# Optimization experiments

Hardware: AMD Instinct MI355X
Metric: run time of the kernel (lower is better)

## Reference

```python
import jax, jax.numpy as jnp
import numpy as np

N = 100_000          # nodes
E = 3_200_000        # edges (avg degree 32)
EMB = 16             # item embedding dim
IN = EMB + 1         # concat(embed, scalar feature)
HID = 32             # GAT hidden size
NEMB = 1000          # embedding vocab
SLOPE = 0.2          # GATConv leaky_relu negative slope


def setup_inputs() -> dict:
    key = jax.random.key(0)
    ks = jax.random.split(key, 24)
    g = lambda k, shape, fan: jax.random.normal(k, shape, dtype=jnp.float32) * (1.0 / np.sqrt(fan))
    inp = {
        "x_ids": jax.random.randint(ks[0], (N,), 0, NEMB, dtype=jnp.int32),
        "x_feat": jax.random.normal(ks[1], (N, 1), dtype=jnp.float32),
        "src": jax.random.randint(ks[2], (E,), 0, N, dtype=jnp.int32),
        "dst": jax.random.randint(ks[3], (E,), 0, N, dtype=jnp.int32),
        "edge_attr": jax.random.normal(ks[4], (E, 1), dtype=jnp.float32),
        # embedding table
        "emb": g(ks[5], (NEMB, EMB), EMB),
        # GATConv 1 (in=17, out=32, heads=1, edge_dim=1)
        "W1": g(ks[6], (IN, HID), IN),
        "a_s1": g(ks[7], (HID,), HID),
        "a_d1": g(ks[8], (HID,), HID),
        "We1": g(ks[9], (1, HID), 1),
        "a_e1": g(ks[10], (HID,), HID),
        "b1": jnp.zeros((HID,), jnp.float32),
        # GATConv 2 (in=32, out=32)
        "W2": g(ks[11], (HID, HID), HID),
        "a_s2": g(ks[12], (HID,), HID),
        "a_d2": g(ks[13], (HID,), HID),
        "We2": g(ks[14], (1, HID), 1),
        "a_e2": g(ks[15], (HID,), HID),
        "b2": jnp.zeros((HID,), jnp.float32),
        # final linear (32 -> 1)
        "lin_w": g(ks[16], (HID, 1), HID),
        "lin_b": jnp.zeros((1,), jnp.float32),
    }
    return inp


def _gat_conv(x, src, dst, eattr, W, a_s, a_d, We, a_e, b):
    """PyG GATConv (heads=1, concat=True) with edge features, self-loops already added."""
    h = x @ W                                   # [N, HID]
    alpha_src = h @ a_s                         # [N]
    alpha_dst = h @ a_d                         # [N]
    alpha_edge = (eattr @ We) @ a_e             # [E']
    alpha = jax.nn.leaky_relu(alpha_src[src] + alpha_dst[dst] + alpha_edge, SLOPE)
    # segment softmax over incoming edges of each dst node
    m = jax.ops.segment_max(alpha, dst, num_segments=N)
    ex = jnp.exp(alpha - m[dst])
    denom = jax.ops.segment_sum(ex, dst, num_segments=N)
    coef = ex / (denom[dst] + 1e-16)
    out = jax.ops.segment_sum(coef[:, None] * h[src], dst, num_segments=N)
    return out + b


def reference(x_ids, x_feat, src, dst, edge_attr, emb,
              W1, a_s1, a_d1, We1, a_e1, b1,
              W2, a_s2, a_d2, We2, a_e2, b2,
              lin_w, lin_b):
    # embedding lookup + concat scalar feature -> [N, 17]
    x = jnp.concatenate([emb[x_ids], x_feat], axis=1)

    # add self-loops once; self-loop edge_attr = mean of incoming edge attrs (fill_value='mean')
    loop = jnp.arange(N, dtype=src.dtype)
    deg = jax.ops.segment_sum(jnp.ones((E,), x.dtype), dst, num_segments=N)
    loop_attr = jax.ops.segment_sum(edge_attr, dst, num_segments=N) / jnp.maximum(deg, 1.0)[:, None]
    src2 = jnp.concatenate([src, loop])
    dst2 = jnp.concatenate([dst, loop])
    ea2 = jnp.concatenate([edge_attr, loop_attr], axis=0)

    x = _gat_conv(x, src2, dst2, ea2, W1, a_s1, a_d1, We1, a_e1, b1)
    x = jax.nn.relu(x)  # dropout is identity in eval mode
    x = _gat_conv(x, src2, dst2, ea2, W2, a_s2, a_d2, We2, a_e2, b2)
    return x @ lin_w + lin_b  # [N, 1]
```

## Files before the change

kernel.cpp:

```cpp
#include <hip/hip_runtime.h>

#define NN 100000
#define EE 3200000
#define SLOPE 0.2f

#define BKN 128
constexpr int NBK = (NN + BKN - 1) / BKN;
#define CAP 4544
constexpr int EP = EE + NN;
#define EPB 4096
constexpr int NBB = (EE + EPB - 1) / EPB;

__global__ void k_bucket(const int* __restrict__ src, const int* __restrict__ dst,
                         const float* __restrict__ ea, int* __restrict__ cnt,
                         int2* __restrict__ stage) {
    __shared__ int hst[NBK];
    __shared__ int scl[NBK];
    __shared__ int gdel[NBK];
    __shared__ int aux[256];
    __shared__ int2 rec[EPB];
    __shared__ int addr[EPB];
    int t = threadIdx.x;
    int base = blockIdx.x * EPB;
    int nedge = min(EPB, EE - base);
    for (int i = t; i < NBK; i += 256) hst[i] = 0;
    __syncthreads();
    int ds[16], ss[16]; float es[16];
#pragma unroll
    for (int j = 0; j < 16; j++) {
        int e = base + j * 256 + t;
        bool v = e < EE;
        ds[j] = v ? dst[e] : -1;
        ss[j] = v ? src[e] : 0;
        es[j] = v ? ea[e] : 0.f;
        if (v) atomicAdd(&hst[ds[j] >> 7], 1);
    }
    __syncthreads();
    int i0 = t * 4;
    int v0 = (i0 + 0 < NBK) ? hst[i0 + 0] : 0;
    int v1 = (i0 + 1 < NBK) ? hst[i0 + 1] : 0;
    int v2 = (i0 + 2 < NBK) ? hst[i0 + 2] : 0;
    int v3 = (i0 + 3 < NBK) ? hst[i0 + 3] : 0;
    int tsum = v0 + v1 + v2 + v3;
    aux[t] = tsum;
    __syncthreads();
    for (int off = 1; off < 256; off <<= 1) {
        int x = (t >= off) ? aux[t - off] : 0;
        __syncthreads();
        aux[t] += x;
        __syncthreads();
    }
    int ex = aux[t] - tsum;
    if (i0 + 0 < NBK) scl[i0 + 0] = ex;
    if (i0 + 1 < NBK) scl[i0 + 1] = ex + v0;
    if (i0 + 2 < NBK) scl[i0 + 2] = ex + v0 + v1;
    if (i0 + 3 < NBK) scl[i0 + 3] = ex + v0 + v1 + v2;
    __syncthreads();
    for (int i = t; i < NBK; i += 256) {
        int h = hst[i];
        int g = h ? atomicAdd(&cnt[i], h) : 0;
        gdel[i] = (g + i * CAP) - scl[i];
    }
    __syncthreads();
#pragma unroll
    for (int j = 0; j < 16; j++) {
        if (ds[j] >= 0) {
            int bk = ds[j] >> 7;
            int pos = atomicAdd(&scl[bk], 1);
            int gpos = pos + gdel[bk];
            rec[pos] = make_int2(ss[j] | ((ds[j] & 127) << 17), __float_as_int(es[j]));
            addr[pos] = (gpos - bk * CAP < CAP) ? gpos : -1;
        }
    }
    __syncthreads();
    for (int i = t; i < nedge; i += 256) {
        int a = addr[i];
        if (a >= 0) stage[a] = rec[i];
    }
}

__global__ void k_scanb(const int* __restrict__ cnt, int* __restrict__ fbase) {
    __shared__ int a[1024];
    int t = threadIdx.x;
    int v = 0;
    if (t < NBK) v = min(cnt[t], CAP) + min(BKN, NN - t * BKN);
    a[t] = v;
    __syncthreads();
    for (int off = 1; off < 1024; off <<= 1) {
        int x = (t >= off) ? a[t - off] : 0;
        __syncthreads();
        a[t] += x;
        __syncthreads();
    }
    if (t < NBK) fbase[t] = a[t] - v;
}

__global__ void k_build(const int* __restrict__ cnt, const int* __restrict__ fbase,
                        const int2* __restrict__ stage, int2* __restrict__ csr,
                        int* __restrict__ offs) {
    __shared__ int ldeg[BKN];
    __shared__ float esum[BKN];
    __shared__ int sc[BKN];
    __shared__ int lcur[BKN];
    int b = blockIdx.x, t = threadIdx.x;
    int nbase = b * BKN;
    int npb = min(BKN, NN - nbase);
    int c = min(cnt[b], CAP);
    const int2* ep = stage + (size_t)b * CAP;
    if (t < BKN) { ldeg[t] = 0; esum[t] = 0.f; }
    __syncthreads();
    for (int i = t; i < c; i += 256) {
        int2 e = ep[i];
        int n = (e.x >> 17) & 127;
        atomicAdd(&ldeg[n], 1);
        atomicAdd(&esum[n], __int_as_float(e.y));
    }
    __syncthreads();
    int v = (t < npb) ? ldeg[t] + 1 : 0;
    if (t < BKN) sc[t] = v;
    __syncthreads();
    for (int off = 1; off < BKN; off <<= 1) {
        int x = (t >= off && t < BKN) ? sc[t - off] : 0;
        __syncthreads();
        if (t < BKN) sc[t] += x;
        __syncthreads();
    }
    if (t < npb) {
        int start = fbase[b] + sc[t] - v;
        offs[nbase + t] = start;
        lcur[t] = start;
    }
    __syncthreads();
    for (int i = t; i < c; i += 256) {
        int2 e = ep[i];
        int n = (e.x >> 17) & 127;
        int pos = atomicAdd(&lcur[n], 1);
        csr[pos] = make_int2(e.x & 0x1FFFF, e.y);
    }
    __syncthreads();
    if (t < npb) {
        float mean = esum[t] / fmaxf((float)ldeg[t], 1.0f);
        csr[lcur[t]] = make_int2(nbase + t, __float_as_int(mean));
    }
    if (b == 0 && t == 0) offs[NN] = EP;
}

__global__ void k_const(const float* __restrict__ We1, const float* __restrict__ ae1,
                        const float* __restrict__ We2, const float* __restrict__ ae2,
                        float* __restrict__ cbuf) {
    int lane = threadIdx.x & 63;
    int comp = lane & 31;
    float p = (lane < 32) ? We1[comp] * ae1[comp] : We2[comp] * ae2[comp];
#pragma unroll
    for (int off = 16; off >= 1; off >>= 1) p += __shfl_xor(p, off);
    if (comp == 0) cbuf[lane >> 5] = p;
}


__global__ void k_h1(const int* __restrict__ ids, const float* __restrict__ feat,
                     const float* __restrict__ emb, const float* __restrict__ W,
                     const float* __restrict__ avs, const float* __restrict__ avd,
                     float* __restrict__ h, float* __restrict__ as_, float* __restrict__ ad_) {
    int n = blockIdx.x * 256 + threadIdx.x;
    if (n >= NN) return;
    float hv[32];
#pragma unroll
    for (int j = 0; j < 32; j++) hv[j] = 0.f;
    int id = ids[n];
    const float4* e4 = (const float4*)(emb + (size_t)id * 16);
#pragma unroll
    for (int k4 = 0; k4 < 4; k4++) {
        float4 xv = e4[k4];
        const float* wr = W + k4 * 4 * 32;
#pragma unroll
        for (int j = 0; j < 32; j++)
            hv[j] += xv.x * wr[j] + xv.y * wr[32 + j] + xv.z * wr[64 + j] + xv.w * wr[96 + j];
    }
    float f = feat[n];
#pragma unroll
    for (int j = 0; j < 32; j++) hv[j] += f * W[16 * 32 + j];
    float s = 0.f, d = 0.f;
#pragma unroll
    for (int j = 0; j < 32; j++) { s += hv[j] * avs[j]; d += hv[j] * avd[j]; }
    as_[n] = s;
    ad_[n] = d;
    float4* h4 = (float4*)(h + (size_t)n * 32);
#pragma unroll
    for (int q = 0; q < 8; q++)
        h4[q] = make_float4(hv[4 * q], hv[4 * q + 1], hv[4 * q + 2], hv[4 * q + 3]);
}

__global__ void k_h2(const float* __restrict__ x, const float* __restrict__ W,
                     const float* __restrict__ avs, const float* __restrict__ avd,
                     float* __restrict__ h, float* __restrict__ as_, float* __restrict__ ad_) {
    int n = blockIdx.x * 256 + threadIdx.x;
    if (n >= NN) return;
    float hv[32];
#pragma unroll
    for (int j = 0; j < 32; j++) hv[j] = 0.f;
    const float4* x4 = (const float4*)(x + (size_t)n * 32);
#pragma unroll
    for (int k4 = 0; k4 < 8; k4++) {
        float4 xv = x4[k4];
        const float* wr = W + k4 * 4 * 32;
#pragma unroll
        for (int j = 0; j < 32; j++)
            hv[j] += xv.x * wr[j] + xv.y * wr[32 + j] + xv.z * wr[64 + j] + xv.w * wr[96 + j];
    }
    float s = 0.f, d = 0.f;
#pragma unroll
    for (int j = 0; j < 32; j++) { s += hv[j] * avs[j]; d += hv[j] * avd[j]; }
    as_[n] = s;
    ad_[n] = d;
    float4* h4 = (float4*)(h + (size_t)n * 32);
#pragma unroll
    for (int q = 0; q < 8; q++)
        h4[q] = make_float4(hv[4 * q], hv[4 * q + 1], hv[4 * q + 2], hv[4 * q + 3]);
}

template <bool FINAL>
__global__ void k_gat(const int* __restrict__ offs, const int2* __restrict__ csr,
                      const float* __restrict__ h, const float* __restrict__ as_,
                      const float* __restrict__ ad_, const float* __restrict__ cbuf,
                      int cidx, const float* __restrict__ bias,
                      const float* __restrict__ lw, const float* __restrict__ lb,
                      float* __restrict__ out) {
    __shared__ int2 xb[4][64];
    int wid = threadIdx.x >> 6;
    int node = blockIdx.x * 4 + wid;
    if (node >= NN) return;
    int lane = threadIdx.x & 63;
    int comp = lane & 31;
    int slot = lane >> 5;
    int base = offs[node];
    int cnt = offs[node + 1] - base;
    float c = cbuf[cidx];
    float adn = ad_[node];
    float acc0 = 0.f, acc1 = 0.f, acc2 = 0.f, acc3 = 0.f, exs = 0.f;
    for (int cb = 0; cb < cnt; cb += 64) {
        int idx = cb + lane;
        bool val = idx < cnt;
        int2 e = csr[base + (val ? idx : 0)];
        int s = e.x;
        float a = as_[s] + adn + c * __int_as_float(e.y);
        a = (a >= 0.f) ? a : SLOPE * a;
        float ex = val ? __expf(a) : 0.f;
        exs += ex;
        xb[wid][lane] = make_int2(s << 5, __float_as_int(ex));
        int m = min(cnt - cb, 64);
        for (int j = 0; j < m; j += 8) {
            int2 p0 = xb[wid][j + slot];
            int2 p1 = xb[wid][j + 2 + slot];
            int2 p2 = xb[wid][j + 4 + slot];
            int2 p3 = xb[wid][j + 6 + slot];
            acc0 += __int_as_float(p0.y) * h[p0.x + comp];
            acc1 += __int_as_float(p1.y) * h[p1.x + comp];
            acc2 += __int_as_float(p2.y) * h[p2.x + comp];
            acc3 += __int_as_float(p3.y) * h[p3.x + comp];
        }
    }
    float acc = (acc0 + acc1) + (acc2 + acc3);
    acc += __shfl_xor(acc, 32);
#pragma unroll
    for (int off = 1; off < 64; off <<= 1) exs += __shfl_xor(exs, off);
    float o = acc / (exs + 1e-16f) + bias[comp];
    if (!FINAL) {
        o = fmaxf(o, 0.f);
        if (lane < 32) out[(size_t)node * 32 + comp] = o;
    } else {
        float y = o * lw[comp];
#pragma unroll
        for (int off = 16; off >= 1; off >>= 1) y += __shfl_xor(y, off);
        if (lane == 0) out[node] = y + lb[0];
    }
}


extern "C" void kernel_launch(void* const* d_in, const int* in_sizes, int n_in,
                              void* d_out, int out_size, void* d_ws, size_t ws_size,
                              hipStream_t stream) {
    const int* x_ids = (const int*)d_in[0];
    const float* x_feat = (const float*)d_in[1];
    const int* src = (const int*)d_in[2];
    const int* dst = (const int*)d_in[3];
    const float* eattr = (const float*)d_in[4];
    const float* emb = (const float*)d_in[5];
    const float* W1 = (const float*)d_in[6];
    const float* a_s1 = (const float*)d_in[7];
    const float* a_d1 = (const float*)d_in[8];
    const float* We1 = (const float*)d_in[9];
    const float* a_e1 = (const float*)d_in[10];
    const float* b1 = (const float*)d_in[11];
    const float* W2 = (const float*)d_in[12];
    const float* a_s2 = (const float*)d_in[13];
    const float* a_d2 = (const float*)d_in[14];
    const float* We2 = (const float*)d_in[15];
    const float* a_e2 = (const float*)d_in[16];
    const float* b2 = (const float*)d_in[17];
    const float* lin_w = (const float*)d_in[18];
    const float* lin_b = (const float*)d_in[19];

    char* p = (char*)d_ws;
    auto alloc = [&](size_t bytes) {
        void* r = (void*)p;
        p += (bytes + 255) & ~(size_t)255;
        return r;
    };
    int* cnt = (int*)alloc(NBK * 4);
    int* fbase = (int*)alloc(NBK * 4);
    float* cbuf = (float*)alloc(2 * 4);
    int* offs = (int*)alloc((NN + 1) * 4);
    float* asb = (float*)alloc(NN * 4);
    float* adb = (float*)alloc(NN * 4);
    int2* csr = (int2*)alloc((size_t)EP * 8);
    void* regionA = alloc((size_t)NBK * CAP * 8);
    int2* stage = (int2*)regionA;
    float* hbuf = (float*)regionA;
    float* x2 = hbuf + (size_t)NN * 32;
    (void)ws_size; (void)in_sizes; (void)n_in; (void)out_size;

    hipMemsetAsync(cnt, 0, NBK * 4, stream);

    const int NBT = (NN + 255) / 256;
    const int NW = (NN + 3) / 4;

    k_bucket<<<NBB, 256, 0, stream>>>(src, dst, eattr, cnt, stage);
    k_scanb<<<1, 1024, 0, stream>>>(cnt, fbase);
    k_build<<<NBK, 256, 0, stream>>>(cnt, fbase, stage, csr, offs);
    k_const<<<1, 64, 0, stream>>>(We1, a_e1, We2, a_e2, cbuf);

    k_h1<<<NBT, 256, 0, stream>>>(x_ids, x_feat, emb, W1, a_s1, a_d1, hbuf, asb, adb);
    k_gat<false><<<NW, 256, 0, stream>>>(offs, csr, hbuf, asb, adb, cbuf, 0, b1,
                                         nullptr, nullptr, x2);
    k_h2<<<NBT, 256, 0, stream>>>(x2, W2, a_s2, a_d2, hbuf, asb, adb);
    k_gat<true><<<NW, 256, 0, stream>>>(offs, csr, hbuf, asb, adb, cbuf, 1, b2,
                                        lin_w, lin_b, (float*)d_out);
}
```

Measured before the change: 352.5 us.

## Fuse node projections into bucketing and GAT kernels, merge small launches

```diff
diff --git a/kernel.cpp b/kernel.cpp
--- a/kernel.cpp
+++ b/kernel.cpp
@@ -10,10 +10,16 @@
 constexpr int EP = EE + NN;
 #define EPB 4096
 constexpr int NBB = (EE + EPB - 1) / EPB;
-
-__global__ void k_bucket(const int* __restrict__ src, const int* __restrict__ dst,
-                         const float* __restrict__ ea, int* __restrict__ cnt,
-                         int2* __restrict__ stage) {
+constexpr int NBT = (NN + 255) / 256;
+
+__global__ void k_fat(const int* __restrict__ src, const int* __restrict__ dst,
+                      const float* __restrict__ ea, int* __restrict__ cnt,
+                      int2* __restrict__ stage,
+                      const int* __restrict__ ids, const float* __restrict__ feat,
+                      const float* __restrict__ emb, const float* __restrict__ W,
+                      const float* __restrict__ avs, const float* __restrict__ avd,
+                      float* __restrict__ h, float* __restrict__ as_,
+                      float* __restrict__ ad_) {
     __shared__ int hst[NBK];
     __shared__ int scl[NBK];
     __shared__ int gdel[NBK];
@@ -21,67 +27,110 @@
     __shared__ int2 rec[EPB];
     __shared__ int addr[EPB];
     int t = threadIdx.x;
-    int base = blockIdx.x * EPB;
-    int nedge = min(EPB, EE - base);
-    for (int i = t; i < NBK; i += 256) hst[i] = 0;
-    __syncthreads();
-    int ds[16], ss[16]; float es[16];
-#pragma unroll
-    for (int j = 0; j < 16; j++) {
-        int e = base + j * 256 + t;
-        bool v = e < EE;
-        ds[j] = v ? dst[e] : -1;
-        ss[j] = v ? src[e] : 0;
-        es[j] = v ? ea[e] : 0.f;
-        if (v) atomicAdd(&hst[ds[j] >> 7], 1);
-    }
-    __syncthreads();
-    int i0 = t * 4;
-    int v0 = (i0 + 0 < NBK) ? hst[i0 + 0] : 0;
-    int v1 = (i0 + 1 < NBK) ? hst[i0 + 1] : 0;
-    int v2 = (i0 + 2 < NBK) ? hst[i0 + 2] : 0;
-    int v3 = (i0 + 3 < NBK) ? hst[i0 + 3] : 0;
-    int tsum = v0 + v1 + v2 + v3;
-    aux[t] = tsum;
-    __syncthreads();
-    for (int off = 1; off < 256; off <<= 1) {
-        int x = (t >= off) ? aux[t - off] : 0;
-        __syncthreads();
-        aux[t] += x;
-        __syncthreads();
-    }
-    int ex = aux[t] - tsum;
-    if (i0 + 0 < NBK) scl[i0 + 0] = ex;
-    if (i0 + 1 < NBK) scl[i0 + 1] = ex + v0;
-    if (i0 + 2 < NBK) scl[i0 + 2] = ex + v0 + v1;
-    if (i0 + 3 < NBK) scl[i0 + 3] = ex + v0 + v1 + v2;
-    __syncthreads();
-    for (int i = t; i < NBK; i += 256) {
-        int h = hst[i];
-        int g = h ? atomicAdd(&cnt[i], h) : 0;
-        gdel[i] = (g + i * CAP) - scl[i];
-    }
-    __syncthreads();
-#pragma unroll
-    for (int j = 0; j < 16; j++) {
-        if (ds[j] >= 0) {
-            int bk = ds[j] >> 7;
-            int pos = atomicAdd(&scl[bk], 1);
-            int gpos = pos + gdel[bk];
-            rec[pos] = make_int2(ss[j] | ((ds[j] & 127) << 17), __float_as_int(es[j]));
-            addr[pos] = (gpos - bk * CAP < CAP) ? gpos : -1;
-        }
-    }
-    __syncthreads();
-    for (int i = t; i < nedge; i += 256) {
-        int a = addr[i];
-        if (a >= 0) stage[a] = rec[i];
-    }
-}
-
-__global__ void k_scanb(const int* __restrict__ cnt, int* __restrict__ fbase) {
+    if (blockIdx.x < NBB) {
+        int base = blockIdx.x * EPB;
+        int nedge = min(EPB, EE - base);
+        for (int i = t; i < NBK; i += 256) hst[i] = 0;
+        __syncthreads();
+        int ds[16], ss[16]; float es[16];
+#pragma unroll
+        for (int j = 0; j < 16; j++) {
+            int e = base + j * 256 + t;
+            bool v = e < EE;
+            ds[j] = v ? dst[e] : -1;
+            ss[j] = v ? src[e] : 0;
+            es[j] = v ? ea[e] : 0.f;
+            if (v) atomicAdd(&hst[ds[j] >> 7], 1);
+        }
+        __syncthreads();
+        int i0 = t * 4;
+        int v0 = (i0 + 0 < NBK) ? hst[i0 + 0] : 0;
+        int v1 = (i0 + 1 < NBK) ? hst[i0 + 1] : 0;
+        int v2 = (i0 + 2 < NBK) ? hst[i0 + 2] : 0;
+        int v3 = (i0 + 3 < NBK) ? hst[i0 + 3] : 0;
+        int tsum = v0 + v1 + v2 + v3;
+        aux[t] = tsum;
+        __syncthreads();
+        for (int off = 1; off < 256; off <<= 1) {
+            int x = (t >= off) ? aux[t - off] : 0;
+            __syncthreads();
+            aux[t] += x;
+            __syncthreads();
+        }
+        int ex = aux[t] - tsum;
+        if (i0 + 0 < NBK) scl[i0 + 0] = ex;
+        if (i0 + 1 < NBK) scl[i0 + 1] = ex + v0;
+        if (i0 + 2 < NBK) scl[i0 + 2] = ex + v0 + v1;
+        if (i0 + 3 < NBK) scl[i0 + 3] = ex + v0 + v1 + v2;
+        __syncthreads();
+        for (int i = t; i < NBK; i += 256) {
+            int hh = hst[i];
+            int g = hh ? atomicAdd(&cnt[i], hh) : 0;
+            gdel[i] = (g + i * CAP) - scl[i];
+        }
+        __syncthreads();
+#pragma unroll
+        for (int j = 0; j < 16; j++) {
+            if (ds[j] >= 0) {
+                int bk = ds[j] >> 7;
+                int pos = atomicAdd(&scl[bk], 1);
+                int gpos = pos + gdel[bk];
+                rec[pos] = make_int2(ss[j] | ((ds[j] & 127) << 17), __float_as_int(es[j]));
+                addr[pos] = (gpos - bk * CAP < CAP) ? gpos : -1;
+            }
+        }
+        __syncthreads();
+        for (int i = t; i < nedge; i += 256) {
+            int a = addr[i];
+            if (a >= 0) stage[a] = rec[i];
+        }
+    } else {
+        int n = (blockIdx.x - NBB) * 256 + t;
+        if (n >= NN) return;
+        float hv[32];
+#pragma unroll
+        for (int j = 0; j < 32; j++) hv[j] = 0.f;
+        int id = ids[n];
+        const float4* e4 = (const float4*)(emb + (size_t)id * 16);
+#pragma unroll
+        for (int k4 = 0; k4 < 4; k4++) {
+            float4 xv = e4[k4];
+            const float* wr = W + k4 * 4 * 32;
+#pragma unroll
+            for (int j = 0; j < 32; j++)
+                hv[j] += xv.x * wr[j] + xv.y * wr[32 + j] + xv.z * wr[64 + j] + xv.w * wr[96 + j];
+        }
+        float f = feat[n];
+#pragma unroll
+        for (int j = 0; j < 32; j++) hv[j] += f * W[16 * 32 + j];
+        float s = 0.f, d = 0.f;
+#pragma unroll
+        for (int j = 0; j < 32; j++) { s += hv[j] * avs[j]; d += hv[j] * avd[j]; }
+        as_[n] = s;
+        ad_[n] = d;
+        float4* h4 = (float4*)(h + (size_t)n * 32);
+#pragma unroll
+        for (int q = 0; q < 8; q++)
+            h4[q] = make_float4(hv[4 * q], hv[4 * q + 1], hv[4 * q + 2], hv[4 * q + 3]);
+    }
+}
+
+__global__ void k_scanc(const int* __restrict__ cnt, int* __restrict__ fbase,
+                        const float* __restrict__ We1, const float* __restrict__ ae1,
+                        const float* __restrict__ We2, const float* __restrict__ ae2,
+                        float* __restrict__ cbuf) {
     __shared__ int a[1024];
     int t = threadIdx.x;
+    if (blockIdx.x == 1) {
+        if (t < 64) {
+            int comp = t & 31;
+            float p = (t < 32) ? We1[comp] * ae1[comp] : We2[comp] * ae2[comp];
+#pragma unroll
+            for (int off = 16; off >= 1; off >>= 1) p += __shfl_xor(p, off);
+            if (comp == 0) cbuf[t >> 5] = p;
+        }
+        return;
+    }
     int v = 0;
     if (t < NBK) v = min(cnt[t], CAP) + min(BKN, NN - t * BKN);
     a[t] = v;
@@ -109,7 +158,7 @@
     const int2* ep = stage + (size_t)b * CAP;
     if (t < BKN) { ldeg[t] = 0; esum[t] = 0.f; }
     __syncthreads();
-    for (int i = t; i < c; i += 256) {
+    for (int i = t; i < c; i += 1024) {
         int2 e = ep[i];
         int n = (e.x >> 17) & 127;
         atomicAdd(&ldeg[n], 1);
@@ -131,7 +180,7 @@
         lcur[t] = start;
     }
     __syncthreads();
-    for (int i = t; i < c; i += 256) {
+    for (int i = t; i < c; i += 1024) {
         int2 e = ep[i];
         int n = (e.x >> 17) & 127;
         int pos = atomicAdd(&lcur[n], 1);
@@ -143,79 +192,6 @@
         csr[lcur[t]] = make_int2(nbase + t, __float_as_int(mean));
     }
     if (b == 0 && t == 0) offs[NN] = EP;
-}
-
-__global__ void k_const(const float* __restrict__ We1, const float* __restrict__ ae1,
-                        const float* __restrict__ We2, const float* __restrict__ ae2,
-                        float* __restrict__ cbuf) {
-    int lane = threadIdx.x & 63;
-    int comp = lane & 31;
-    float p = (lane < 32) ? We1[comp] * ae1[comp] : We2[comp] * ae2[comp];
-#pragma unroll
-    for (int off = 16; off >= 1; off >>= 1) p += __shfl_xor(p, off);
-    if (comp == 0) cbuf[lane >> 5] = p;
-}
-
-
-__global__ void k_h1(const int* __restrict__ ids, const float* __restrict__ feat,
-                     const float* __restrict__ emb, const float* __restrict__ W,
-                     const float* __restrict__ avs, const float* __restrict__ avd,
-                     float* __restrict__ h, float* __restrict__ as_, float* __restrict__ ad_) {
-    int n = blockIdx.x * 256 + threadIdx.x;
-    if (n >= NN) return;
-    float hv[32];
-#pragma unroll
-    for (int j = 0; j < 32; j++) hv[j] = 0.f;
-    int id = ids[n];
-    const float4* e4 = (const float4*)(emb + (size_t)id * 16);
-#pragma unroll
-    for (int k4 = 0; k4 < 4; k4++) {
-        float4 xv = e4[k4];
-        const float* wr = W + k4 * 4 * 32;
-#pragma unroll
-        for (int j = 0; j < 32; j++)
-            hv[j] += xv.x * wr[j] + xv.y * wr[32 + j] + xv.z * wr[64 + j] + xv.w * wr[96 + j];
-    }
-    float f = feat[n];
-#pragma unroll
-    for (int j = 0; j < 32; j++) hv[j] += f * W[16 * 32 + j];
-    float s = 0.f, d = 0.f;
-#pragma unroll
-    for (int j = 0; j < 32; j++) { s += hv[j] * avs[j]; d += hv[j] * avd[j]; }
-    as_[n] = s;
-    ad_[n] = d;
-    float4* h4 = (float4*)(h + (size_t)n * 32);
-#pragma unroll
-    for (int q = 0; q < 8; q++)
-        h4[q] = make_float4(hv[4 * q], hv[4 * q + 1], hv[4 * q + 2], hv[4 * q + 3]);
-}
-
-__global__ void k_h2(const float* __restrict__ x, const float* __restrict__ W,
-                     const float* __restrict__ avs, const float* __restrict__ avd,
-                     float* __restrict__ h, float* __restrict__ as_, float* __restrict__ ad_) {
-    int n = blockIdx.x * 256 + threadIdx.x;
-    if (n >= NN) return;
-    float hv[32];
-#pragma unroll
-    for (int j = 0; j < 32; j++) hv[j] = 0.f;
-    const float4* x4 = (const float4*)(x + (size_t)n * 32);
-#pragma unroll
-    for (int k4 = 0; k4 < 8; k4++) {
-        float4 xv = x4[k4];
-        const float* wr = W + k4 * 4 * 32;
-#pragma unroll
-        for (int j = 0; j < 32; j++)
-            hv[j] += xv.x * wr[j] + xv.y * wr[32 + j] + xv.z * wr[64 + j] + xv.w * wr[96 + j];
-    }
-    float s = 0.f, d = 0.f;
-#pragma unroll
-    for (int j = 0; j < 32; j++) { s += hv[j] * avs[j]; d += hv[j] * avd[j]; }
-    as_[n] = s;
-    ad_[n] = d;
-    float4* h4 = (float4*)(h + (size_t)n * 32);
-#pragma unroll
-    for (int q = 0; q < 8; q++)
-        h4[q] = make_float4(hv[4 * q], hv[4 * q + 1], hv[4 * q + 2], hv[4 * q + 3]);
 }
 
 template <bool FINAL>
@@ -223,20 +199,29 @@
                       const float* __restrict__ h, const float* __restrict__ as_,
                       const float* __restrict__ ad_, const float* __restrict__ cbuf,
                       int cidx, const float* __restrict__ bias,
+                      const float* __restrict__ W2, const float* __restrict__ avs2,
+                      const float* __restrict__ avd2, float* __restrict__ h2,
+                      float* __restrict__ as2, float* __restrict__ ad2,
                       const float* __restrict__ lw, const float* __restrict__ lb,
                       float* __restrict__ out) {
     __shared__ int2 xb[4][64];
-    int wid = threadIdx.x >> 6;
+    __shared__ float w2s[1024];
+    int t = threadIdx.x;
+    if (!FINAL) {
+        for (int i = t; i < 1024; i += 256) w2s[i] = W2[i];
+        __syncthreads();
+    }
+    int wid = t >> 6;
     int node = blockIdx.x * 4 + wid;
-    if (node >= NN) return;
-    int lane = threadIdx.x & 63;
-    int comp = lane & 31;
-    int slot = lane >> 5;
+    int lane = t & 63;
+    int comp = t & 31;
+    int slot = (t >> 5) & 1;
     int base = offs[node];
     int cnt = offs[node + 1] - base;
     float c = cbuf[cidx];
     float adn = ad_[node];
-    float acc0 = 0.f, acc1 = 0.f, acc2 = 0.f, acc3 = 0.f, exs = 0.f;
+    float a0 = 0.f, a1 = 0.f, a2 = 0.f, a3 = 0.f;
+    float a4 = 0.f, a5 = 0.f, a6 = 0.f, a7 = 0.f, exs = 0.f;
     for (int cb = 0; cb < cnt; cb += 64) {
         int idx = cb + lane;
         bool val = idx < cnt;
@@ -248,25 +233,45 @@
         exs += ex;
         xb[wid][lane] = make_int2(s << 5, __float_as_int(ex));
         int m = min(cnt - cb, 64);
-        for (int j = 0; j < m; j += 8) {
-            int2 p0 = xb[wid][j + slot];
-            int2 p1 = xb[wid][j + 2 + slot];
-            int2 p2 = xb[wid][j + 4 + slot];
-            int2 p3 = xb[wid][j + 6 + slot];
-            acc0 += __int_as_float(p0.y) * h[p0.x + comp];
-            acc1 += __int_as_float(p1.y) * h[p1.x + comp];
-            acc2 += __int_as_float(p2.y) * h[p2.x + comp];
-            acc3 += __int_as_float(p3.y) * h[p3.x + comp];
-        }
-    }
-    float acc = (acc0 + acc1) + (acc2 + acc3);
+        for (int j = 0; j < m; j += 16) {
+            int2 q0 = xb[wid][j + slot];
+            int2 q1 = xb[wid][j + 2 + slot];
+            int2 q2 = xb[wid][j + 4 + slot];
+            int2 q3 = xb[wid][j + 6 + slot];
+            int2 q4 = xb[wid][j + 8 + slot];
+            int2 q5 = xb[wid][j + 10 + slot];
+            int2 q6 = xb[wid][j + 12 + slot];
+            int2 q7 = xb[wid][j + 14 + slot];
+            a0 += __int_as_float(q0.y) * h[q0.x + comp];
+            a1 += __int_as_float(q1.y) * h[q1.x + comp];
+            a2 += __int_as_float(q2.y) * h[q2.x + comp];
+            a3 += __int_as_float(q3.y) * h[q3.x + comp];
+            a4 += __int_as_float(q4.y) * h[q4.x + comp];
+            a5 += __int_as_float(q5.y) * h[q5.x + comp];
+            a6 += __int_as_float(q6.y) * h[q6.x + comp];
+            a7 += __int_as_float(q7.y) * h[q7.x + comp];
+        }
+    }
+    float acc = ((a0 + a1) + (a2 + a3)) + ((a4 + a5) + (a6 + a7));
     acc += __shfl_xor(acc, 32);
 #pragma unroll
     for (int off = 1; off < 64; off <<= 1) exs += __shfl_xor(exs, off);
     float o = acc / (exs + 1e-16f) + bias[comp];
     if (!FINAL) {
         o = fmaxf(o, 0.f);
-        if (lane < 32) out[(size_t)node * 32 + comp] = o;
+        float hv = 0.f;
+#pragma unroll
+        for (int k = 0; k < 32; k++)
+            hv += __shfl(o, k, 32) * w2s[k * 32 + comp];
+        if (lane < 32) h2[(size_t)node * 32 + comp] = hv;
+        float ps = hv * avs2[comp];
+        float pd = hv * avd2[comp];
+#pragma unroll
+        for (int off = 16; off >= 1; off >>= 1) {
+            ps += __shfl_xor(ps, off);
+            pd += __shfl_xor(pd, off);
+        }
+        if (lane == 0) { as2[node] = ps; ad2[node] = pd; }
     } else {
         float y = o * lw[comp];
 #pragma unroll
@@ -310,29 +315,30 @@
     int* fbase = (int*)alloc(NBK * 4);
     float* cbuf = (float*)alloc(2 * 4);
     int* offs = (int*)alloc((NN + 1) * 4);
-    float* asb = (float*)alloc(NN * 4);
-    float* adb = (float*)alloc(NN * 4);
+    float* asb1 = (float*)alloc(NN * 4);
+    float* adb1 = (float*)alloc(NN * 4);
+    float* h1 = (float*)alloc((size_t)NN * 32 * 4);
     int2* csr = (int2*)alloc((size_t)EP * 8);
-    void* regionA = alloc((size_t)NBK * CAP * 8);
+    char* regionA = (char*)alloc((size_t)NBK * CAP * 8);
     int2* stage = (int2*)regionA;
-    float* hbuf = (float*)regionA;
-    float* x2 = hbuf + (size_t)NN * 32;
+    float* h2 = (float*)regionA;
+    float* asb2 = (float*)(regionA + (size_t)NN * 32 * 4);
+    float* adb2 = asb2 + NN;
     (void)ws_size; (void)in_sizes; (void)n_in; (void)out_size;
 
     hipMemsetAsync(cnt, 0, NBK * 4, stream);
 
-    const int NBT = (NN + 255) / 256;
     const int NW = (NN + 3) / 4;
 
-    k_bucket<<<NBB, 256, 0, stream>>>(src, dst, eattr, cnt, stage);
-    k_scanb<<<1, 1024, 0, stream>>>(cnt, fbase);
-    k_build<<<NBK, 256, 0, stream>>>(cnt, fbase, stage, csr, offs);
-    k_const<<<1, 64, 0, stream>>>(We1, a_e1, We2, a_e2, cbuf);
-
-    k_h1<<<NBT, 256, 0, stream>>>(x_ids, x_feat, emb, W1, a_s1, a_d1, hbuf, asb, adb);
-    k_gat<false><<<NW, 256, 0, stream>>>(offs, csr, hbuf, asb, adb, cbuf, 0, b1,
-                                         nullptr, nullptr, x2);
-    k_h2<<<NBT, 256, 0, stream>>>(x2, W2, a_s2, a_d2, hbuf, asb, adb);
-    k_gat<true><<<NW, 256, 0, stream>>>(offs, csr, hbuf, asb, adb, cbuf, 1, b2,
-                                        lin_w, lin_b, (float*)d_out);
-}
+    k_fat<<<NBB + NBT, 256, 0, stream>>>(src, dst, eattr, cnt, stage,
+                                         x_ids, x_feat, emb, W1, a_s1, a_d1,
+                                         h1, asb1, adb1);
+    k_scanc<<<2, 1024, 0, stream>>>(cnt, fbase, We1, a_e1, We2, a_e2, cbuf);
+    k_build<<<NBK, 1024, 0, stream>>>(cnt, fbase, stage, csr, offs);
+    k_gat<false><<<NW, 256, 0, stream>>>(offs, csr, h1, asb1, adb1, cbuf, 0, b1,
+                                         W2, a_s2, a_d2, h2, asb2, adb2,
+                                         nullptr, nullptr, nullptr);
+    k_gat<true><<<NW, 256, 0, stream>>>(offs, csr, h2, asb2, adb2, cbuf, 1, b2,
+                                        nullptr, nullptr, nullptr, nullptr, nullptr,
+                                        nullptr, lin_w, lin_b, (float*)d_out);
+}
```

After: 342.3 us. -2.9%, faster.
